# Performance work log

Hardware: AMD Instinct MI355X
Metric: run time of the kernel (lower is better)

The kernel has to match this reference:

```python
import jax, jax.numpy as jnp
import numpy as np

B, P, N, D = 32, 100, 1000, 128
SQRT_D = 11.313708498984761
CLIP = 10.0


def setup_inputs() -> dict:
    key = jax.random.key(0)
    ks = jax.random.split(key, 8)
    s = 1.0 / np.sqrt(D)  # keep k ~ N(0,1) so exp(k) is stable
    return {
        "encoded_nodes": jax.random.normal(ks[0], (B, N, D), jnp.float32),
        "encoded_q1": jax.random.normal(ks[1], (B, P, D), jnp.float32),
        "encoded_last_node": jax.random.normal(ks[2], (B, P, D), jnp.float32),
        "cur_dist": jax.random.uniform(ks[3], (B, P, N), jnp.float32),
        "ninf_mask": jnp.zeros((B, P, N), jnp.float32),
        "log_scale": jnp.ones((1,), jnp.float32),
        "Wq_first": jax.random.normal(ks[4], (D, D), jnp.float32) * s,
        "Wq_last": jax.random.normal(ks[5], (D, D), jnp.float32) * s,
        "Wk": jax.random.normal(ks[6], (D, D), jnp.float32) * s,
        "Wv": jax.random.normal(ks[7], (D, D), jnp.float32) * s,
        "dist_alpha_1": jnp.ones((1,), jnp.float32),
        "AFT_dist_alpha_1": jnp.ones((1,), jnp.float32),
    }


def reference(encoded_nodes, encoded_q1, encoded_last_node, cur_dist, ninf_mask,
              log_scale, Wq_first, Wq_last, Wk, Wv, dist_alpha_1, AFT_dist_alpha_1):
    # set_kv / set_q1 (torch Linear: x @ W.T)
    k = jnp.einsum('bnd,ed->bne', encoded_nodes, Wk)          # [B,N,D]
    v = jnp.einsum('bnd,ed->bne', encoded_nodes, Wv)          # [B,N,D]
    q_first = jnp.einsum('bpd,ed->bpe', encoded_q1, Wq_first) # [B,P,D]
    q_last = jnp.einsum('bpd,ed->bpe', encoded_last_node, Wq_last)
    q = q_first + q_last

    cur_dist_out = -cur_dist                                   # [B,P,N]
    bias_scale = log_scale * AFT_dist_alpha_1 * cur_dist_out + ninf_mask
    ebias = jnp.exp(bias_scale)                                # [B,P,N]
    ek = jnp.exp(k)                                            # [B,N,D]
    num = jnp.einsum('bpn,bnd->bpd', ebias, ek * v)
    den = jnp.einsum('bpn,bnd->bpd', ebias, ek)
    aft_out = jax.nn.sigmoid(q) * (num / den)                  # [B,P,D]

    score = jnp.einsum('bpd,bnd->bpn', aft_out, encoded_nodes) / SQRT_D
    score = score + log_scale * dist_alpha_1 * cur_dist_out
    score = CLIP * jnp.tanh(score) + ninf_mask
    return jax.nn.softmax(score, axis=2)
```

## Files before the change

### kernel.cpp

```cpp
#include <hip/hip_runtime.h>
#include <hip/hip_bf16.h>
#include <math.h>

#define B 32
#define P 100
#define N 1000
#define D 128

constexpr float SQRT_D_INV = 1.0f / 11.313708498984761f;
constexpr float CLIPV = 10.0f;

__device__ __forceinline__ void fma4(float4& a, float s, const float4& b) {
    a.x = fmaf(s, b.x, a.x);
    a.y = fmaf(s, b.y, a.y);
    a.z = fmaf(s, b.z, a.z);
    a.w = fmaf(s, b.w, a.w);
}

#define GLDS(gsrc, ldst) __builtin_amdgcn_global_load_lds( \
    (const __attribute__((address_space(1))) void*)(gsrc), \
    (__attribute__((address_space(3))) void*)(ldst), 16, 0, 0)

#define TT 64
__global__ __launch_bounds__(256) void prep_kernel(
        const float* __restrict__ nodes,
        const float* __restrict__ Wk,  const float* __restrict__ Wv,
        const float* __restrict__ Wqf, const float* __restrict__ Wql,
        float* __restrict__ wkT,  float* __restrict__ wvT,
        float* __restrict__ wqfT, float* __restrict__ wqlT,
        float* __restrict__ nodesT) {
    const int t = threadIdx.x;
    if (blockIdx.x < D) {
        const int e = blockIdx.x;
        const int d = t & 127;
        if ((t >> 7) == 0) {
            wkT[e * D + d] = Wk[d * D + e];
            wvT[e * D + d] = Wv[d * D + e];
        } else {
            wqfT[e * D + d] = Wqf[d * D + e];
            wqlT[e * D + d] = Wql[d * D + e];
        }
        return;
    }
    __shared__ float sh[TT][D + 1];
    const int blk = blockIdx.x - D;
    const int ntiles = (N + TT - 1) / TT;
    const int b  = blk / ntiles;
    const int n0 = (blk % ntiles) * TT;
    const int rows = min(TT, N - n0);

    const float4* src = (const float4*)(nodes + ((long)b * N + n0) * D);
    for (int i = t; i < rows * (D / 4); i += 256) {
        int r = i >> 5, c = i & 31;
        float4 v = src[(long)r * (D / 4) + c];
        sh[r][c * 4 + 0] = v.x; sh[r][c * 4 + 1] = v.y;
        sh[r][c * 4 + 2] = v.z; sh[r][c * 4 + 3] = v.w;
    }
    __syncthreads();

    const int nl = t & 63;
    const int eg = t >> 6;
    if (nl < rows) {
        #pragma unroll
        for (int k = 0; k < 32; ++k) {
            int e = eg * 32 + k;
            nodesT[((long)b * D + e) * N + n0 + nl] = sh[nl][e];
        }
    }
}

#define R1 64
#define CH 8
__global__ __launch_bounds__(512) void kv_kernel(
        const float* __restrict__ nodes,
        const float* __restrict__ wkT,
        const float* __restrict__ wvT,
        float* __restrict__ ek,
        float* __restrict__ ekv) {
    __shared__ float sh[R1][D];
    __shared__ __align__(16) float wL[2][2][CH * D];
    const int t = threadIdx.x;
    const int lane = t & 63;
    const int wid = t >> 6;
    const int dq = t & 31;
    const int rl = t >> 5;
    const long row0 = (long)blockIdx.x * R1;

    const float4* src = (const float4*)(nodes + row0 * D);
    float4* dst = (float4*)(&sh[0][0]);
    #pragma unroll
    for (int i = 0; i < (R1 * D / 4) / 512; ++i)
        dst[t + i * 512] = src[t + i * 512];

    {
        const int seg = wid & 3;
        const float* g = (wid < 4 ? wkT : wvT) + seg * 256 + lane * 4;
        GLDS(g, &wL[0][wid < 4 ? 0 : 1][seg * 256]);
    }
    __syncthreads();

    float4 ka[4], va[4];
    #pragma unroll
    for (int rr = 0; rr < 4; ++rr) {
        ka[rr] = make_float4(0.f, 0.f, 0.f, 0.f);
        va[rr] = make_float4(0.f, 0.f, 0.f, 0.f);
    }

    int buf = 0;
    for (int c = 0; c < D / CH; ++c) {
        if (c + 1 < D / CH) {
            const int seg = wid & 3;
            const float* g = (wid < 4 ? wkT : wvT)
                           + (long)(c + 1) * CH * D + seg * 256 + lane * 4;
            GLDS(g, &wL[buf ^ 1][wid < 4 ? 0 : 1][seg * 256]);
        }

        const float* wkb = &wL[buf][0][dq * 4];
        const float* wvb = &wL[buf][1][dq * 4];
        #pragma unroll
        for (int ee0 = 0; ee0 < CH; ee0 += 4) {
            float4 cwk[4], cwv[4];
            #pragma unroll
            for (int ee = 0; ee < 4; ++ee) {
                cwk[ee] = *(const float4*)(wkb + (ee0 + ee) * D);
                cwv[ee] = *(const float4*)(wvb + (ee0 + ee) * D);
            }
            const int e0 = c * CH + ee0;
            #pragma unroll
            for (int rr = 0; rr < 4; ++rr) {
                float4 s4 = *(const float4*)(&sh[rl * 4 + rr][e0]);
                fma4(ka[rr], s4.x, cwk[0]); fma4(ka[rr], s4.y, cwk[1]);
                fma4(ka[rr], s4.z, cwk[2]); fma4(ka[rr], s4.w, cwk[3]);
                fma4(va[rr], s4.x, cwv[0]); fma4(va[rr], s4.y, cwv[1]);
                fma4(va[rr], s4.z, cwv[2]); fma4(va[rr], s4.w, cwv[3]);
            }
        }
        __syncthreads();
        buf ^= 1;
    }

    #pragma unroll
    for (int rr = 0; rr < 4; ++rr) {
        long row = row0 + rl * 4 + rr;
        float4 e4;
        e4.x = __expf(ka[rr].x); e4.y = __expf(ka[rr].y);
        e4.z = __expf(ka[rr].z); e4.w = __expf(ka[rr].w);
        float4 ev;
        ev.x = e4.x * va[rr].x; ev.y = e4.y * va[rr].y;
        ev.z = e4.z * va[rr].z; ev.w = e4.w * va[rr].w;
        *(float4*)(ek + row * D + dq * 4) = e4;
        *(float4*)(ekv + row * D + dq * 4) = ev;
    }
}

#define R2 16
__global__ __launch_bounds__(256) void q_kernel(
        const float* __restrict__ q1,
        const float* __restrict__ qlast,
        const float* __restrict__ wqfT,
        const float* __restrict__ wqlT,
        float* __restrict__ qsig) {
    __shared__ float sh1[R2][D];
    __shared__ float sh2[R2][D];
    const int t = threadIdx.x;
    const int dq = t & 31;
    const int rl = t >> 5;
    const long row0 = (long)blockIdx.x * R2;

    const float4* s1 = (const float4*)(q1 + row0 * D);
    const float4* s2 = (const float4*)(qlast + row0 * D);
    float4* d1 = (float4*)(&sh1[0][0]);
    float4* d2 = (float4*)(&sh2[0][0]);
    #pragma unroll
    for (int i = 0; i < (R2 * D / 4) / 256; ++i) {
        d1[t + i * 256] = s1[t + i * 256];
        d2[t + i * 256] = s2[t + i * 256];
    }
    __syncthreads();

    float4 acc[2];
    acc[0] = make_float4(0.f, 0.f, 0.f, 0.f);
    acc[1] = make_float4(0.f, 0.f, 0.f, 0.f);

    const float* wfp = wqfT + dq * 4;
    const float* wlp = wqlT + dq * 4;

    float4 cwf[4], cwl[4];
    #pragma unroll
    for (int ee = 0; ee < 4; ++ee) {
        cwf[ee] = *(const float4*)(wfp + ee * D);
        cwl[ee] = *(const float4*)(wlp + ee * D);
    }

    for (int e0 = 0; e0 < D; e0 += 4) {
        float4 nwf[4], nwl[4];
        if (e0 + 4 < D) {
            #pragma unroll
            for (int ee = 0; ee < 4; ++ee) {
                nwf[ee] = *(const float4*)(wfp + (e0 + 4 + ee) * D);
                nwl[ee] = *(const float4*)(wlp + (e0 + 4 + ee) * D);
            }
        }
        #pragma unroll
        for (int rr = 0; rr < 2; ++rr) {
            float4 a4 = *(const float4*)(&sh1[rl * 2 + rr][e0]);
            float4 b4 = *(const float4*)(&sh2[rl * 2 + rr][e0]);
            fma4(acc[rr], a4.x, cwf[0]); fma4(acc[rr], a4.y, cwf[1]);
            fma4(acc[rr], a4.z, cwf[2]); fma4(acc[rr], a4.w, cwf[3]);
            fma4(acc[rr], b4.x, cwl[0]); fma4(acc[rr], b4.y, cwl[1]);
            fma4(acc[rr], b4.z, cwl[2]); fma4(acc[rr], b4.w, cwl[3]);
        }
        #pragma unroll
        for (int ee = 0; ee < 4; ++ee) { cwf[ee] = nwf[ee]; cwl[ee] = nwl[ee]; }
    }

    #pragma unroll
    for (int rr = 0; rr < 2; ++rr) {
        long row = row0 + rl * 2 + rr;
        float4 s;
        s.x = 1.0f / (1.0f + __expf(-acc[rr].x));
        s.y = 1.0f / (1.0f + __expf(-acc[rr].y));
        s.z = 1.0f / (1.0f + __expf(-acc[rr].z));
        s.w = 1.0f / (1.0f + __expf(-acc[rr].w));
        *(float4*)(qsig + row * D + dq * 4) = s;
    }
}

#define PT3 50
#define TS 32
#define EBC 57
__global__ __launch_bounds__(256) void aft_part_kernel(
        const float* __restrict__ cur_dist,
        const float* __restrict__ ninf,
        const float* __restrict__ ek,
        const float* __restrict__ ekv,
        const float* __restrict__ log_scale,
        const float* __restrict__ aft_alpha,
        float* __restrict__ pnum,
        float* __restrict__ pden,
        int NC, int L) {
    __shared__ float eb[2][TS][EBC];
    const int t = threadIdx.x;
    const int dq = t & 31;
    const int pg = t >> 5;
    const int pbase = pg * 7;
    const int phys = blockIdx.x;
    const int g    = (phys >> 4) * 8 + (phys & 7);
    const int pt   = (phys >> 3) & 1;
    const int b    = g % B;
    const int c    = g / B;
    const int p0 = pt * PT3;
    const int n_begin = c * L;
    const int n_end = min(N, n_begin + L);
    const float lsA = log_scale[0] * aft_alpha[0];

    float4 num[7], den[7];
    #pragma unroll
    for (int i = 0; i < 7; ++i) {
        num[i] = make_float4(0.f, 0.f, 0.f, 0.f);
        den[i] = make_float4(0.f, 0.f, 0.f, 0.f);
    }

    float rv[7];
    int n0 = n_begin;
    int ts = min(TS, n_end - n0);

    #pragma unroll
    for (int k = 0; k < 7; ++k) {
        int s = t + k * 256;
        int pp = s >> 5, nl = s & 31;
        rv[k] = 0.f;
        if (nl < ts && p0 + pp < P) {
            long idx = ((long)b * P + p0 + pp) * N + (n0 + nl);
            rv[k] = fmaf(-lsA, cur_dist[idx], ninf[idx]);
        }
    }

    int buf = 0;
    while (n0 < n_end) {
        #pragma unroll
        for (int k = 0; k < 7; ++k) {
            int s = t + k * 256;
            int pp = s >> 5, nl = s & 31;
            if (nl < ts) eb[buf][nl][pp] = __expf(rv[k]);
        }
        __syncthreads();

        const int n0n = n0 + ts;
        const int tsn = min(TS, n_end - n0n);
        if (n0n < n_end) {
            #pragma unroll
            for (int k = 0; k < 7; ++k) {
                int s = t + k * 256;
                int pp = s >> 5, nl = s & 31;
                rv[k] = 0.f;
                if (nl < tsn && p0 + pp < P) {
                    long idx = ((long)b * P + p0 + pp) * N + (n0n + nl);
                    rv[k] = fmaf(-lsA, cur_dist[idx], ninf[idx]);
                }
            }
        }

        const float* ekb = ek  + ((long)b * N + n0) * D + dq * 4;
        const float* evb = ekv + ((long)b * N + n0) * D + dq * 4;
        #pragma unroll 4
        for (int j = 0; j < ts; ++j) {
            float4 ekq = *(const float4*)(ekb + (long)j * D);
            float4 evq = *(const float4*)(evb + (long)j * D);
            float e0 = eb[buf][j][pbase + 0];
            float e1 = eb[buf][j][pbase + 1];
            float e2 = eb[buf][j][pbase + 2];
            float e3 = eb[buf][j][pbase + 3];
            float e4 = eb[buf][j][pbase + 4];
            float e5 = eb[buf][j][pbase + 5];
            float e6 = eb[buf][j][pbase + 6];
            fma4(num[0], e0, evq); fma4(den[0], e0, ekq);
            fma4(num[1], e1, evq); fma4(den[1], e1, ekq);
            fma4(num[2], e2, evq); fma4(den[2], e2, ekq);
            fma4(num[3], e3, evq); fma4(den[3], e3, ekq);
            fma4(num[4], e4, evq); fma4(den[4], e4, ekq);
            fma4(num[5], e5, evq); fma4(den[5], e5, ekq);
            fma4(num[6], e6, evq); fma4(den[6], e6, ekq);
        }
        buf ^= 1;
        n0 = n0n;
        ts = tsn;
    }

    #pragma unroll
    for (int r = 0; r < 7; ++r) {
        int pl_ = pbase + r;
        if (pl_ < PT3) {
            int p = p0 + pl_;
            long o = (((long)c * B + b) * P + p) * D + dq * 4;
            *(float4*)(pnum + o) = num[r];
            *(float4*)(pden + o) = den[r];
        }
    }
}

__global__ __launch_bounds__(256) void aft_reduce_kernel(
        const float* __restrict__ pnum,
        const float* __restrict__ pden,
        const float* __restrict__ qsig,
        float* __restrict__ aft,
        int NC) {
    const long i = ((long)blockIdx.x * 256 + threadIdx.x) * 4;
    const long BPD = (long)B * P * D;
    float4 n = make_float4(0.f, 0.f, 0.f, 0.f);
    float4 d = make_float4(0.f, 0.f, 0.f, 0.f);
    int c = 0;
    for (; c + 2 <= NC; c += 2) {
        float4 a0 = *(const float4*)(pnum + (long)c * BPD + i);
        float4 a1 = *(const float4*)(pnum + (long)(c + 1) * BPD + i);
        float4 b0 = *(const float4*)(pden + (long)c * BPD + i);
        float4 b1 = *(const float4*)(pden + (long)(c + 1) * BPD + i);
        n.x += a0.x + a1.x; n.y += a0.y + a1.y;
        n.z += a0.z + a1.z; n.w += a0.w + a1.w;
        d.x += b0.x + b1.x; d.y += b0.y + b1.y;
        d.z += b0.z + b1.z; d.w += b0.w + b1.w;
    }
    if (c < NC) {
        float4 a0 = *(const float4*)(pnum + (long)c * BPD + i);
        float4 b0 = *(const float4*)(pden + (long)c * BPD + i);
        n.x += a0.x; n.y += a0.y; n.z += a0.z; n.w += a0.w;
        d.x += b0.x; d.y += b0.y; d.z += b0.z; d.w += b0.w;
    }
    float4 q = *(const float4*)(qsig + i);
    float4 o;
    o.x = q.x * n.x / d.x;
    o.y = q.y * n.y / d.y;
    o.z = q.z * n.z / d.z;
    o.w = q.w * n.w / d.w;
    *(float4*)(aft + i) = o;
}

#define PT2 10
#define SC 4
__global__ __launch_bounds__(128) void score_part_kernel(
        const float* __restrict__ aft,
        const float* __restrict__ nodesT,
        const float* __restrict__ cur_dist,
        const float* __restrict__ ninf,
        const float* __restrict__ log_scale,
        const float* __restrict__ dist_alpha,
        float* __restrict__ out,
        float* __restrict__ sums) {
    __shared__ float sa[PT2][D];
    __shared__ float red[2][PT2];
    const int t = threadIdx.x;
    const int wid = t >> 6;
    const int b    = blockIdx.x % B;
    const int rest = blockIdx.x / B;
    const int c    = rest % SC;
    const int pt   = rest / SC;
    const int p0 = pt * PT2;
    const float lsA = log_scale[0] * dist_alpha[0];

    for (int i = t; i < PT2 * D; i += 128) {
        sa[i >> 7][i & 127] = aft[((long)b * P + p0) * D + i];
    }
    __syncthreads();

    const int n0 = c * 256 + t * 2;
    const bool act = (n0 < N);
    const int ncl = act ? n0 : 0;
    const float* ntb = nodesT + (long)b * D * N;

    float2 acc[PT2];
    #pragma unroll
    for (int i = 0; i < PT2; ++i) acc[i] = make_float2(0.f, 0.f);

    float2 cx[4];
    #pragma unroll
    for (int ee = 0; ee < 4; ++ee)
        cx[ee] = *(const float2*)(ntb + (long)ee * N + ncl);

    for (int e0 = 0; e0 < D; e0 += 4) {
        float2 nx[4];
        if (e0 + 4 < D) {
            #pragma unroll
            for (int ee = 0; ee < 4; ++ee)
                nx[ee] = *(const float2*)(ntb + (long)(e0 + 4 + ee) * N + ncl);
        }
        #pragma unroll
        for (int i = 0; i < PT2; ++i) {
            float4 a4 = *(const float4*)(&sa[i][e0]);
            acc[i].x = fmaf(cx[0].x, a4.x, acc[i].x);
            acc[i].x = fmaf(cx[1].x, a4.y, acc[i].x);
            acc[i].x = fmaf(cx[2].x, a4.z, acc[i].x);
            acc[i].x = fmaf(cx[3].x, a4.w, acc[i].x);
            acc[i].y = fmaf(cx[0].y, a4.x, acc[i].y);
            acc[i].y = fmaf(cx[1].y, a4.y, acc[i].y);
            acc[i].y = fmaf(cx[2].y, a4.z, acc[i].y);
            acc[i].y = fmaf(cx[3].y, a4.w, acc[i].y);
        }
        #pragma unroll
        for (int ee = 0; ee < 4; ++ee) cx[ee] = nx[ee];
    }

    #pragma unroll
    for (int i = 0; i < PT2; ++i) {
        float2 ev = make_float2(0.f, 0.f);
        if (act) {
            long idx = ((long)b * P + p0 + i) * N + n0;
            float2 cd = *(const float2*)(cur_dist + idx);
            float2 nf = *(const float2*)(ninf + idx);
            float sx = fmaf(acc[i].x, SQRT_D_INV, -lsA * cd.x);
            float sy = fmaf(acc[i].y, SQRT_D_INV, -lsA * cd.y);
            float ax = fabsf(sx), ay = fabsf(sy);
            float rx = 1.f - 2.f / (__expf(2.f * ax) + 1.f);
            float ry = 1.f - 2.f / (__expf(2.f * ay) + 1.f);
            float scx = CLIPV * copysignf(rx, sx) + nf.x;
            float scy = CLIPV * copysignf(ry, sy) + nf.y;
            ev.x = __expf(scx);
            ev.y = __expf(scy);
            *(float2*)(out + idx) = ev;
        }
        float s = ev.x + ev.y;
        #pragma unroll
        for (int o = 1; o < 64; o <<= 1) s += __shfl_xor(s, o, 64);
        if ((t & 63) == 0) red[wid][i] = s;
    }
    __syncthreads();
    if (t < PT2) {
        atomicAdd(&sums[b * P + p0 + t], red[0][t] + red[1][t]);
    }
}

__global__ __launch_bounds__(256) void normalize_kernel(
        float* __restrict__ out, const float* __restrict__ sums) {
    const int row = blockIdx.x;
    const int t = threadIdx.x;
    const float inv = 1.0f / sums[row];
    float4* r = (float4*)(out + (long)row * N);
    if (t < N / 4) {
        float4 v = r[t];
        v.x *= inv; v.y *= inv; v.z *= inv; v.w *= inv;
        r[t] = v;
    }
}

extern "C" void kernel_launch(void* const* d_in, const int* in_sizes, int n_in,
                              void* d_out, int out_size, void* d_ws, size_t ws_size,
                              hipStream_t stream) {
    const float* nodes      = (const float*)d_in[0];
    const float* q1         = (const float*)d_in[1];
    const float* qlast      = (const float*)d_in[2];
    const float* cur_dist   = (const float*)d_in[3];
    const float* ninf       = (const float*)d_in[4];
    const float* log_scale  = (const float*)d_in[5];
    const float* Wqf        = (const float*)d_in[6];
    const float* Wql        = (const float*)d_in[7];
    const float* Wk         = (const float*)d_in[8];
    const float* Wv         = (const float*)d_in[9];
    const float* dist_alpha = (const float*)d_in[10];
    const float* aft_alpha  = (const float*)d_in[11];
    float* out = (float*)d_out;

    const long BND = (long)B * N * D;
    const long BPD = (long)B * P * D;
    const long W2  = (long)D * D;

    float* ws     = (float*)d_ws;
    float* ek     = ws;
    float* ekv    = ek + BND;
    float* qsig   = ekv + BND;
    float* aft    = qsig + BPD;
    float* wkT    = aft + BPD;
    float* wvT    = wkT + W2;
    float* wqfT   = wvT + W2;
    float* wqlT   = wqfT + W2;
    float* nodesT = wqlT + W2;
    float* sums   = nodesT + BND;
    float* pnum   = sums + (long)B * P;

    long avail = (long)(ws_size / 4) - (3 * BND + 2 * BPD + 4 * W2 + (long)B * P);
    int NC = (int)(avail / (2 * BPD));
    if (NC < 1) NC = 1;
    if (NC > 16) NC = 16;
    int L = (N + NC - 1) / NC;
    NC = (N + L - 1) / L;
    float* pden = pnum + (long)NC * BPD;

    hipMemsetAsync(sums, 0, (size_t)B * P * sizeof(float), stream);
    prep_kernel<<<D + B * ((N + TT - 1) / TT), 256, 0, stream>>>(
        nodes, Wk, Wv, Wqf, Wql, wkT, wvT, wqfT, wqlT, nodesT);
    kv_kernel<<<(B * N) / R1, 512, 0, stream>>>(nodes, wkT, wvT, ek, ekv);
    q_kernel<<<(B * P) / R2, 256, 0, stream>>>(q1, qlast, wqfT, wqlT, qsig);
    aft_part_kernel<<<B * 2 * NC, 256, 0, stream>>>(
        cur_dist, ninf, ek, ekv, log_scale, aft_alpha, pnum, pden, NC, L);
    aft_reduce_kernel<<<(int)(BPD / 1024), 256, 0, stream>>>(pnum, pden, qsig, aft, NC);
    score_part_kernel<<<B * SC * (P / PT2), 128, 0, stream>>>(
        aft, nodesT, cur_dist, ninf, log_scale, dist_alpha, out, sums);
    normalize_kernel<<<B * P, 256, 0, stream>>>(out, sums);
}
```

Before: 234.9 us.

## Stage ek/ekv tiles into LDS with double-buffered global_load_lds in AFT partial kernel

The AFT partial-sum kernel now copies the ek and ek*v rows for each n-tile into shared memory with asynchronous global-to-LDS loads, double-buffered so the next tile's copy overlaps the current tile's FMAs. Previously every p-group of threads read the same rows straight from global memory. The tile size drops from 32 to 16 rows to fit the larger LDS footprint, the exp-bias buffer becomes single-buffered with an extra barrier per tile, and the per-chunk length L is rounded up to a multiple of 16. The gain is less redundant global/L1 traffic, paid for with more barriers and tiles, and higher LDS use that may reduce occupancy.

```diff
diff --git a/kernel.cpp b/kernel.cpp
--- a/kernel.cpp
+++ b/kernel.cpp
@@ -227,7 +227,7 @@
 }
 
 #define PT3 50
-#define TS 32
+#define TS3 16
 #define EBC 57
 __global__ __launch_bounds__(256) void aft_part_kernel(
         const float* __restrict__ cur_dist,
@@ -239,7 +239,9 @@
         float* __restrict__ pnum,
         float* __restrict__ pden,
         int NC, int L) {
-    __shared__ float eb[2][TS][EBC];
+    __shared__ float eb[TS3][EBC];
+    __shared__ __align__(16) float ekL[2][TS3 * D];
+    __shared__ __align__(16) float evL[2][TS3 * D];
     const int t = threadIdx.x;
     const int dq = t & 31;
     const int pg = t >> 5;
@@ -261,59 +263,76 @@
         den[i] = make_float4(0.f, 0.f, 0.f, 0.f);
     }
 
-    float rv[7];
+    const float* ekc = ek  + (long)b * N * D;
+    const float* evc = ekv + (long)b * N * D;
+
     int n0 = n_begin;
-    int ts = min(TS, n_end - n0);
-
-    #pragma unroll
-    for (int k = 0; k < 7; ++k) {
+    int ts = min(TS3, n_end - n0);
+
+    {
+        const float* gk = ekc + (long)n0 * D;
+        const float* gv = evc + (long)n0 * D;
+        for (int i = t; i < ts * 32; i += 256) {
+            GLDS(gk + (long)i * 4, &ekL[0][i * 4]);
+            GLDS(gv + (long)i * 4, &evL[0][i * 4]);
+        }
+    }
+    float rv[4];
+    #pragma unroll
+    for (int k = 0; k < 4; ++k) {
         int s = t + k * 256;
-        int pp = s >> 5, nl = s & 31;
+        int pp = s >> 4, nl = s & 15;
         rv[k] = 0.f;
-        if (nl < ts && p0 + pp < P) {
+        if (pp < 56 && nl < ts && p0 + pp < P) {
             long idx = ((long)b * P + p0 + pp) * N + (n0 + nl);
             rv[k] = fmaf(-lsA, cur_dist[idx], ninf[idx]);
         }
     }
 
-    int buf = 0;
+    int cur = 0;
     while (n0 < n_end) {
         #pragma unroll
-        for (int k = 0; k < 7; ++k) {
+        for (int k = 0; k < 4; ++k) {
             int s = t + k * 256;
-            int pp = s >> 5, nl = s & 31;
-            if (nl < ts) eb[buf][nl][pp] = __expf(rv[k]);
+            int pp = s >> 4, nl = s & 15;
+            if (pp < 56 && nl < ts) eb[nl][pp] = __expf(rv[k]);
         }
         __syncthreads();
 
         const int n0n = n0 + ts;
-        const int tsn = min(TS, n_end - n0n);
+        const int tsn = min(TS3, n_end - n0n);
         if (n0n < n_end) {
+            const float* gk = ekc + (long)n0n * D;
+            const float* gv = evc + (long)n0n * D;
+            for (int i = t; i < tsn * 32; i += 256) {
+                GLDS(gk + (long)i * 4, &ekL[cur ^ 1][i * 4]);
+                GLDS(gv + (long)i * 4, &evL[cur ^ 1][i * 4]);
+            }
             #pragma unroll
-            for (int k = 0; k < 7; ++k) {
+            for (int k = 0; k < 4; ++k) {
                 int s = t + k * 256;
-                int pp = s >> 5, nl = s & 31;
+                int pp = s >> 4, nl = s & 15;
                 rv[k] = 0.f;
-                if (nl < tsn && p0 + pp < P) {
+                if (pp < 56 && nl < tsn && p0 + pp < P) {
                     long idx = ((long)b * P + p0 + pp) * N + (n0n + nl);
                     rv[k] = fmaf(-lsA, cur_dist[idx], ninf[idx]);
                 }
             }
         }
 
-        const float* ekb = ek  + ((long)b * N + n0) * D + dq * 4;
-        const float* evb = ekv + ((long)b * N + n0) * D + dq * 4;
+        const float* ekp = &ekL[cur][dq * 4];
+        const float* evp = &evL[cur][dq * 4];
         #pragma unroll 4
         for (int j = 0; j < ts; ++j) {
-            float4 ekq = *(const float4*)(ekb + (long)j * D);
-            float4 evq = *(const float4*)(evb + (long)j * D);
-            float e0 = eb[buf][j][pbase + 0];
-            float e1 = eb[buf][j][pbase + 1];
-            float e2 = eb[buf][j][pbase + 2];
-            float e3 = eb[buf][j][pbase + 3];
-            float e4 = eb[buf][j][pbase + 4];
-            float e5 = eb[buf][j][pbase + 5];
-            float e6 = eb[buf][j][pbase + 6];
+            float4 ekq = *(const float4*)(ekp + j * D);
+            float4 evq = *(const float4*)(evp + j * D);
+            float e0 = eb[j][pbase + 0];
+            float e1 = eb[j][pbase + 1];
+            float e2 = eb[j][pbase + 2];
+            float e3 = eb[j][pbase + 3];
+            float e4 = eb[j][pbase + 4];
+            float e5 = eb[j][pbase + 5];
+            float e6 = eb[j][pbase + 6];
             fma4(num[0], e0, evq); fma4(den[0], e0, ekq);
             fma4(num[1], e1, evq); fma4(den[1], e1, ekq);
             fma4(num[2], e2, evq); fma4(den[2], e2, ekq);
@@ -322,7 +341,8 @@
             fma4(num[5], e5, evq); fma4(den[5], e5, ekq);
             fma4(num[6], e6, evq); fma4(den[6], e6, ekq);
         }
-        buf ^= 1;
+        __syncthreads();
+        cur ^= 1;
         n0 = n0n;
         ts = tsn;
     }
@@ -519,7 +539,7 @@
     int NC = (int)(avail / (2 * BPD));
     if (NC < 1) NC = 1;
     if (NC > 16) NC = 16;
-    int L = (N + NC - 1) / NC;
+    int L = (((N + NC - 1) / NC) + 15) & ~15;
     NC = (N + L - 1) / L;
     float* pden = pnum + (long)NC * BPD;
 
```

New measurement: 232.9 us. No clear change (-0.9%).
